# Performance work log

Measured on AMD Instinct MI355X. Metric: run time of the kernel, lower is better.

## Reference

```python
import jax, jax.numpy as jnp
import numpy as np

B, H, W, C = 2, 64, 64, 192
DM = int(2.0 * C)   # d_inner = ssm_ratio * hidden_dim = 384
N = 16              # d_state
R = 12              # dt_rank = ceil(C / 16)
K = 4               # scan directions


def _ln(x, g, b, eps):
    mu = jnp.mean(x, axis=-1, keepdims=True)
    var = jnp.var(x, axis=-1, keepdims=True)
    return (x - mu) * jax.lax.rsqrt(var + eps) * g + b


def setup_inputs() -> dict:
    key = jax.random.key(0)
    ks = jax.random.split(key, 8)
    return {
        "input": jax.random.normal(ks[0], (B, H, W, C), jnp.float32),
        "norm_g": jnp.ones((C,), jnp.float32),
        "norm_b": jnp.zeros((C,), jnp.float32),
        "in_proj_w": jax.random.normal(ks[1], (C, 2 * DM), jnp.float32) * 0.02,
        "conv_w": jax.random.normal(ks[2], (DM, 1, 3, 3), jnp.float32) * 0.1,
        "conv_b": jnp.zeros((DM,), jnp.float32),
        "x_proj_w": jax.random.normal(ks[3], (K, R + 2 * N, DM), jnp.float32) * 0.02,
        "dt_w": jax.random.normal(ks[4], (K, DM, R), jnp.float32) * 0.1,
        "dt_b": jax.random.uniform(ks[5], (K, DM), jnp.float32, -4.0, -2.0),
        "A_logs": jnp.tile(jnp.log(jnp.arange(1, N + 1, dtype=jnp.float32))[None, None, :], (K, DM, 1)),
        "Ds": jnp.ones((K, DM), jnp.float32),
        "out_norm_g": jnp.ones((DM,), jnp.float32),
        "out_norm_b": jnp.zeros((DM,), jnp.float32),
        "out_proj_w": jax.random.normal(ks[6], (DM, C), jnp.float32) * 0.02,
    }


def _selective_scan(us, deltas, A, Bs, Cs):
    # us, deltas: (B,K,D,L); A: (K,D,N); Bs, Cs: (B,K,N,L)
    u_l = jnp.moveaxis(us, -1, 0)       # (L,B,K,D)
    d_l = jnp.moveaxis(deltas, -1, 0)   # (L,B,K,D)
    B_l = jnp.moveaxis(Bs, -1, 0)       # (L,B,K,N)
    C_l = jnp.moveaxis(Cs, -1, 0)       # (L,B,K,N)
    h0 = jnp.zeros(us.shape[:3] + (A.shape[-1],), us.dtype)  # (B,K,D,N)

    def step(h, xs):
        u_t, d_t, b_t, c_t = xs
        dA = jnp.exp(d_t[..., None] * A)                       # (B,K,D,N)
        h = dA * h + (d_t * u_t)[..., None] * b_t[:, :, None, :]
        y = jnp.einsum('bkdn,bkn->bkd', h, c_t)
        return h, y

    _, ys = jax.lax.scan(step, h0, (u_l, d_l, B_l, C_l))
    return jnp.moveaxis(ys, 0, -1)  # (B,K,D,L)


def reference(input, norm_g, norm_b, in_proj_w, conv_w, conv_b, x_proj_w,
              dt_w, dt_b, A_logs, Ds, out_norm_g, out_norm_b, out_proj_w):
    Bz, Hh, Ww, Cc = input.shape
    L = Hh * Ww
    # pre-norm
    xn = _ln(input, norm_g, norm_b, 1e-6)
    # input projection -> x, z
    xz = xn @ in_proj_w                      # (B,H,W,2*DM)
    x, z = jnp.split(xz, 2, axis=-1)
    # depthwise conv + SiLU (channels-first)
    x = jnp.transpose(x, (0, 3, 1, 2))       # (B,DM,H,W)
    Dm = x.shape[1]
    x = jax.lax.conv_general_dilated(
        x, conv_w, (1, 1), 'SAME',
        dimension_numbers=('NCHW', 'OIHW', 'NCHW'),
        feature_group_count=Dm) + conv_b[None, :, None, None]
    x = jax.nn.silu(x)
    # 4-direction cross-scan: hw, wh, and their reverses
    x_flat = x.reshape(Bz, Dm, L)
    x_t = jnp.transpose(x, (0, 1, 3, 2)).reshape(Bz, Dm, L)
    xs = jnp.stack([x_flat, x_t], axis=1)                  # (B,2,DM,L)
    xs = jnp.concatenate([xs, jnp.flip(xs, -1)], axis=1)   # (B,4,DM,L)
    Rr = dt_w.shape[2]
    Nn = A_logs.shape[2]
    x_dbl = jnp.einsum('bkdl,kcd->bkcl', xs, x_proj_w)     # (B,4,R+2N,L)
    dts, Bs, Cs = jnp.split(x_dbl, [Rr, Rr + Nn], axis=2)
    deltas = jax.nn.softplus(
        jnp.einsum('bkrl,kdr->bkdl', dts, dt_w) + dt_b[None, :, :, None])
    A = -jnp.exp(A_logs)                                   # (4,DM,N)
    out_y = _selective_scan(xs, deltas, A, Bs, Cs) + Ds[None, :, :, None] * xs
    # merge the 4 directions back
    inv = jnp.flip(out_y[:, 2:], -1)

    def wh(t):
        return jnp.transpose(t.reshape(Bz, Dm, Ww, Hh), (0, 1, 3, 2)).reshape(Bz, Dm, L)

    y = out_y[:, 0] + inv[:, 0] + wh(out_y[:, 1]) + wh(inv[:, 1])  # (B,DM,L)
    y = jnp.transpose(y, (0, 2, 1))                                # (B,L,DM)
    y = _ln(y, out_norm_g, out_norm_b, 1e-5).reshape(Bz, Hh, Ww, Dm)
    y = y * jax.nn.silu(z)
    out = y @ out_proj_w
    # residual (drop_path=0 -> identity)
    return input + out
```

## Files before the change

kernel.cpp:

```cpp
#include <hip/hip_runtime.h>
#include <hip/hip_bf16.h>
#include <hip/hip_fp16.h>


typedef __attribute__((ext_vector_type(8))) short short8;
typedef __attribute__((ext_vector_type(4))) float floatx4;

__global__ __launch_bounds__(256) void k_ln(const float* __restrict__ in,
                                            const float* __restrict__ g,
                                            const float* __restrict__ be,
                                            __hip_bfloat16* __restrict__ out) {
  int row = blockIdx.x * 4 + (threadIdx.x >> 6);
  int lane = threadIdx.x & 63;
  const float* x = in + (long)row * 192;
  float v0 = x[lane], v1 = x[lane + 64], v2 = x[lane + 128];
  float s = v0 + v1 + v2;
  float s2 = v0 * v0 + v1 * v1 + v2 * v2;
  #pragma unroll
  for (int o = 32; o > 0; o >>= 1) { s += __shfl_xor(s, o); s2 += __shfl_xor(s2, o); }
  float mu = s * (1.f / 192.f);
  float var = s2 * (1.f / 192.f) - mu * mu;
  float r = rsqrtf(var + 1e-6f);
  __hip_bfloat16* op = out + (long)row * 192;
  op[lane]       = __float2bfloat16((v0 - mu) * r * g[lane]       + be[lane]);
  op[lane + 64]  = __float2bfloat16((v1 - mu) * r * g[lane + 64]  + be[lane + 64]);
  op[lane + 128] = __float2bfloat16((v2 - mu) * r * g[lane + 128] + be[lane + 128]);
}

__global__ __launch_bounds__(256) void k_packw(const float* __restrict__ ipw,
                                               const float* __restrict__ xpw,
                                               const float* __restrict__ opw,
                                               __hip_bfloat16* __restrict__ Wt1,
                                               __hip_bfloat16* __restrict__ Wt2,
                                               __hip_bfloat16* __restrict__ Wt3) {
  int idx = blockIdx.x * 256 + threadIdx.x;
  if (idx < 147456) {
    int n = idx / 192, k = idx - n * 192;
    Wt1[idx] = __float2bfloat16(ipw[(long)k * 768 + n]);
  } else if (idx < 147456 + 73728) {
    int t = idx - 147456;
    int j = t / 384;
    float v = (j < 176) ? xpw[t] : 0.f;
    Wt2[t] = __float2bfloat16(v);
  } else if (idx < 147456 + 73728 + 73728) {
    int t = idx - 147456 - 73728;
    int n = t / 384, k = t - n * 384;
    Wt3[t] = __float2bfloat16(opw[(long)k * 192 + n]);
  }
}

__device__ __forceinline__ int inv_dir(int k, int p) {
  int pt = ((p & 63) << 6) | (p >> 6);
  if (k == 0) return p;
  if (k == 1) return pt;
  if (k == 2) return 4095 - p;
  return 4095 - pt;
}
__device__ __forceinline__ int dir_pix(int k, int l) { return inv_dir(k, l); }

template <int EPI>
__global__ __launch_bounds__(256) void k_gemm_mfma(const __hip_bfloat16* __restrict__ A,
                                                   const __hip_bfloat16* __restrict__ Bt,
                                                   const float* __restrict__ Res,
                                                   float* __restrict__ Co,
                                                   __hip_bfloat16* __restrict__ CoB,
                                                   __hip_bfloat16* __restrict__ Co2B,
                                                   float* __restrict__ dtsS,
                                                   float* __restrict__ BsS,
                                                   float* __restrict__ CsS,
                                                   int M, int N, int Kk) {
  __shared__ __align__(16) short As[64 * 64];
  __shared__ __align__(16) short Bs[64 * 64];
  int tid = threadIdx.x;
  int wave = tid >> 6, lane = tid & 63;
  int mlane = lane & 15, quad = lane >> 4;
  int row0 = blockIdx.y * 64, col0 = blockIdx.x * 64;
  int wr = wave & 1, wc = wave >> 1;
  floatx4 acc[2][2];
  #pragma unroll
  for (int mi = 0; mi < 2; mi++)
    #pragma unroll
    for (int ni = 0; ni < 2; ni++) acc[mi][ni] = (floatx4){0.f, 0.f, 0.f, 0.f};

  for (int k0 = 0; k0 < Kk; k0 += 64) {
    #pragma unroll
    for (int c = tid; c < 512; c += 256) {
      int r = c >> 3, j = c & 7;
      *(float4*)&As[r * 64 + ((j ^ (r & 7)) << 3)] =
          *(const float4*)&A[(long)(row0 + r) * Kk + k0 + j * 8];
    }
    #pragma unroll
    for (int c = tid; c < 512; c += 256) {
      int r = c >> 3, j = c & 7;
      *(float4*)&Bs[r * 64 + ((j ^ (r & 7)) << 3)] =
          *(const float4*)&Bt[(long)(col0 + r) * Kk + k0 + j * 8];
    }
    __syncthreads();
    short8 af[2][2], bf[2][2];
    #pragma unroll
    for (int mi = 0; mi < 2; mi++) {
      int r = wr * 32 + mi * 16 + mlane;
      #pragma unroll
      for (int kk = 0; kk < 2; kk++) {
        int jx = (kk * 4 + quad) ^ (r & 7);
        af[mi][kk] = *(const short8*)&As[r * 64 + jx * 8];
      }
    }
    #pragma unroll
    for (int ni = 0; ni < 2; ni++) {
      int rn = wc * 32 + ni * 16 + mlane;
      #pragma unroll
      for (int kk = 0; kk < 2; kk++) {
        int jx = (kk * 4 + quad) ^ (rn & 7);
        bf[ni][kk] = *(const short8*)&Bs[rn * 64 + jx * 8];
      }
    }
    #pragma unroll
    for (int kk = 0; kk < 2; kk++)
      #pragma unroll
      for (int mi = 0; mi < 2; mi++)
        #pragma unroll
        for (int ni = 0; ni < 2; ni++)
          acc[mi][ni] = __builtin_amdgcn_mfma_f32_16x16x32_bf16(af[mi][kk], bf[ni][kk],
                                                                acc[mi][ni], 0, 0, 0);
    __syncthreads();
  }
  #pragma unroll
  for (int mi = 0; mi < 2; mi++) {
    #pragma unroll
    for (int ni = 0; ni < 2; ni++) {
      int cc = col0 + wc * 32 + ni * 16 + mlane;
      #pragma unroll
      for (int i = 0; i < 4; i++) {
        int rr = row0 + wr * 32 + mi * 16 + quad * 4 + i;
        float v = acc[mi][ni][i];
        if (EPI == 1) {
          Co[(long)rr * N + cc] = v + Res[(long)rr * N + cc];
        } else if (EPI == 2) {
          if (cc < 384) CoB[(long)rr * 384 + cc] = __float2bfloat16(v);
          else          Co2B[(long)rr * 384 + (cc - 384)] = __float2bfloat16(v);
        } else {
          if (cc < 176) {
            int k4 = (cc >= 132) ? 3 : (cc >= 88) ? 2 : (cc >= 44) ? 1 : 0;
            int c = cc - k4 * 44;
            int b = rr >> 12, p = rr & 4095;
            long lbase = ((long)((b << 2) + k4) << 12) + p;
            if (c < 12)      dtsS[lbase * 12 + c] = v;
            else if (c < 28) BsS[lbase * 16 + (c - 12)] = v;
            else             CsS[lbase * 16 + (c - 28)] = v;
          }
        }
      }
    }
  }
}

__global__ __launch_bounds__(384) void k_conv(const __hip_bfloat16* __restrict__ xbufB,
                                              const float* __restrict__ cw,
                                              const float* __restrict__ cb,
                                              __hip_bfloat16* __restrict__ xcb) {
  int row = blockIdx.x;
  int b = row >> 12, p = row & 4095;
  int h = p >> 6, w0 = p & 63;
  int d = threadIdx.x;
  float acc = cb[d];
  const float* wt = cw + d * 9;
  #pragma unroll
  for (int dh = -1; dh <= 1; dh++) {
    int hh = h + dh;
    if (hh < 0 || hh > 63) continue;
    #pragma unroll
    for (int dw = -1; dw <= 1; dw++) {
      int ww = w0 + dw;
      if (ww < 0 || ww > 63) continue;
      acc += __bfloat162float(xbufB[((long)(b << 12) + (hh << 6) + ww) * 384 + d])
             * wt[(dh + 1) * 3 + (dw + 1)];
    }
  }
  float sg = 1.f / (1.f + __expf(-acc));
  xcb[(long)row * 384 + d] = __float2bfloat16(acc * sg);
}

__global__ __launch_bounds__(384) void k_dt(const float* __restrict__ dtsS,
                                            const float* __restrict__ dt_w,
                                            const float* __restrict__ dt_b,
                                            __half* __restrict__ dpre) {
  int bid = blockIdx.x;
  int chunk = bid & 127, bk = bid >> 7;
  int k = bk & 3;
  int d = threadIdx.x;
  float w[12];
  const float* dwp = dt_w + ((long)(k * 384) + d) * 12;
  #pragma unroll
  for (int r = 0; r < 12; r++) w[r] = dwp[r];
  float db = dt_b[k * 384 + d];
  long base = ((long)bk << 12) + chunk * 32;
  #pragma unroll 4
  for (int t = 0; t < 32; t++) {
    const float4* dq = (const float4*)(dtsS + (base + t) * 12);
    float4 q0 = dq[0], q1 = dq[1], q2 = dq[2];
    float x = db + q0.x * w[0] + q0.y * w[1] + q0.z * w[2] + q0.w * w[3]
                 + q1.x * w[4] + q1.y * w[5] + q1.z * w[6] + q1.w * w[7]
                 + q2.x * w[8] + q2.y * w[9] + q2.z * w[10] + q2.w * w[11];
    float e = __expf(x);
    float delta = (x > 15.f) ? x : __logf(1.f + e);
    dpre[(base + t) * 384 + d] = __float2half(delta);
  }
}

__device__ __forceinline__ void pow16(float r, float* pws) {
  pws[0] = r;
  #pragma unroll
  for (int n = 1; n < 16; n++) {
    int m = n + 1, c = (m + 1) / 2, f = m - c;
    pws[n] = pws[c - 1] * pws[f - 1];
  }
}

__global__ __launch_bounds__(384) void k_scan0(
    const __half* __restrict__ dpre, const float* __restrict__ BsS,
    const __hip_bfloat16* __restrict__ xcb,
    const float* __restrict__ A_logs,
    float* __restrict__ Eb, float* __restrict__ Dend) {
  int bid = blockIdx.x;
  int s = bid & 127, bk = bid >> 7;
  int k = bk & 3, b = bk >> 2;
  int d = threadIdx.x;
  const float* al = A_logs + ((long)(k * 384) + d) * 16;
  bool pw = true;
  float av[16];
  #pragma unroll
  for (int n = 0; n < 16; n++) {
    float a = __expf(al[n]);
    av[n] = -a;
    pw = pw && (fabsf(a - (float)(n + 1)) < 1e-3f);
  }
  float h[16];
  #pragma unroll
  for (int n = 0; n < 16; n++) h[n] = 0.f;
  float cum = 0.f;
  long bpk = (long)bk << 12;
  long bpix = (long)(b << 12);

  if (pw) {
    #pragma unroll 4
    for (int t = 0; t < 32; t++) {
      int p = dir_pix(k, s * 32 + t);
      float delta = __half2float(dpre[(bpk + p) * 384 + d]);
      cum += delta;
      float u = __bfloat162float(xcb[(bpix + p) * 384 + d]);
      float du = delta * u;
      float rr = __expf(-delta);
      float pws[16]; pow16(rr, pws);
      const float4* Bq = (const float4*)(BsS + (bpk + p) * 16);
      float4 b0 = Bq[0], b1 = Bq[1], b2 = Bq[2], b3 = Bq[3];
      float Bl[16] = {b0.x, b0.y, b0.z, b0.w, b1.x, b1.y, b1.z, b1.w,
                      b2.x, b2.y, b2.z, b2.w, b3.x, b3.y, b3.z, b3.w};
      #pragma unroll
      for (int n = 0; n < 16; n++) h[n] = pws[n] * h[n] + du * Bl[n];
    }
  } else {
    for (int t = 0; t < 32; t++) {
      int p = dir_pix(k, s * 32 + t);
      float delta = __half2float(dpre[(bpk + p) * 384 + d]);
      cum += delta;
      float u = __bfloat162float(xcb[(bpix + p) * 384 + d]);
      float du = delta * u;
      const float4* Bq = (const float4*)(BsS + (bpk + p) * 16);
      float4 b0 = Bq[0], b1 = Bq[1], b2 = Bq[2], b3 = Bq[3];
      float Bl[16] = {b0.x, b0.y, b0.z, b0.w, b1.x, b1.y, b1.z, b1.w,
                      b2.x, b2.y, b2.z, b2.w, b3.x, b3.y, b3.z, b3.w};
      #pragma unroll
      for (int n = 0; n < 16; n++) {
        float dA = __expf(delta * av[n]);
        h[n] = dA * h[n] + du * Bl[n];
      }
    }
  }
  long g = (long)bk * 128 + s;
  float* Ep = Eb + g * 6144 + d * 16;
  #pragma unroll
  for (int n = 0; n < 16; n++) Ep[n] = h[n];
  Dend[g * 384 + d] = cum;
}

__global__ __launch_bounds__(128) void k_combine(float* __restrict__ Eb,
                                                 const float* __restrict__ Dend,
                                                 const float* __restrict__ A_logs) {
  int bid = blockIdx.x;
  int bk = bid / 384;
  int d = bid - bk * 384;
  int k = bk & 3;
  int s = threadIdx.x;
  const float* al = A_logs + ((long)(k * 384) + d) * 16;
  bool pw = true;
  float av[16];
  #pragma unroll
  for (int n = 0; n < 16; n++) {
    float a = __expf(al[n]);
    av[n] = -a;
    pw = pw && (fabsf(a - (float)(n + 1)) < 1e-3f);
  }

  long ebase = ((long)bk * 128 + s) * 6144 + d * 16;
  float e[16];
  *(float4*)&e[0]  = *(const float4*)&Eb[ebase + 0];
  *(float4*)&e[4]  = *(const float4*)&Eb[ebase + 4];
  *(float4*)&e[8]  = *(const float4*)&Eb[ebase + 8];
  *(float4*)&e[12] = *(const float4*)&Eb[ebase + 12];
  float sig = Dend[((long)bk * 128 + s) * 384 + d];

  __shared__ float sE[128][17];
  sE[s][0] = sig;
  #pragma unroll
  for (int n = 0; n < 16; n++) sE[s][1 + n] = e[n];
  __syncthreads();

  for (int o = 1; o < 128; o <<= 1) {
    float ps = 0.f, pe[16];
    bool act = (s >= o);
    if (act) {
      ps = sE[s - o][0];
      #pragma unroll
      for (int n = 0; n < 16; n++) pe[n] = sE[s - o][1 + n];
    }
    __syncthreads();
    if (act) {
      if (pw) {
        float rc = __expf(-sig);
        float pwr[16]; pow16(rc, pwr);
        #pragma unroll
        for (int n = 0; n < 16; n++) e[n] += pwr[n] * pe[n];
      } else {
        #pragma unroll
        for (int n = 0; n < 16; n++) e[n] += __expf(av[n] * sig) * pe[n];
      }
      sig += ps;
      sE[s][0] = sig;
      #pragma unroll
      for (int n = 0; n < 16; n++) sE[s][1 + n] = e[n];
    }
    __syncthreads();
  }

  float ho[16];
  if (s == 0) {
    #pragma unroll
    for (int n = 0; n < 16; n++) ho[n] = 0.f;
  } else {
    #pragma unroll
    for (int n = 0; n < 16; n++) ho[n] = sE[s - 1][1 + n];
  }
  *(float4*)&Eb[ebase + 0]  = *(float4*)&ho[0];
  *(float4*)&Eb[ebase + 4]  = *(float4*)&ho[4];
  *(float4*)&Eb[ebase + 8]  = *(float4*)&ho[8];
  *(float4*)&Eb[ebase + 12] = *(float4*)&ho[12];
}

template <int ATOMIC>
__global__ __launch_bounds__(384) void k_scan1(
    const __half* __restrict__ dpre, const float* __restrict__ BsS,
    const float* __restrict__ CsS, const __hip_bfloat16* __restrict__ xcb,
    const float* __restrict__ A_logs, const float* __restrict__ Eb,
    float* __restrict__ yout) {
  int bid = blockIdx.x;
  int s = bid & 127, bk = bid >> 7;
  int k = bk & 3, b = bk >> 2;
  int d = threadIdx.x;
  const float* al = A_logs + ((long)(k * 384) + d) * 16;
  bool pw = true;
  float av[16];
  #pragma unroll
  for (int n = 0; n < 16; n++) {
    float a = __expf(al[n]);
    av[n] = -a;
    pw = pw && (fabsf(a - (float)(n + 1)) < 1e-3f);
  }
  float h[16];
  const float* hp = Eb + ((long)bk * 128 + s) * 6144 + d * 16;
  #pragma unroll
  for (int n = 0; n < 16; n++) h[n] = hp[n];
  long bpk = (long)bk << 12;
  long bpix = (long)(b << 12);

  if (pw) {
    #pragma unroll 4
    for (int t = 0; t < 32; t++) {
      int p = dir_pix(k, s * 32 + t);
      float delta = __half2float(dpre[(bpk + p) * 384 + d]);
      float u = __bfloat162float(xcb[(bpix + p) * 384 + d]);
      float du = delta * u;
      float rr = __expf(-delta);
      float pws[16]; pow16(rr, pws);
      const float4* Bq = (const float4*)(BsS + (bpk + p) * 16);
      float4 b0 = Bq[0], b1 = Bq[1], b2 = Bq[2], b3 = Bq[3];
      float Bl[16] = {b0.x, b0.y, b0.z, b0.w, b1.x, b1.y, b1.z, b1.w,
                      b2.x, b2.y, b2.z, b2.w, b3.x, b3.y, b3.z, b3.w};
      const float4* Cq = (const float4*)(CsS + (bpk + p) * 16);
      float4 c0 = Cq[0], c1 = Cq[1], c2 = Cq[2], c3 = Cq[3];
      float Cl[16] = {c0.x, c0.y, c0.z, c0.w, c1.x, c1.y, c1.z, c1.w,
                      c2.x, c2.y, c2.z, c2.w, c3.x, c3.y, c3.z, c3.w};
      float y = 0.f;
      #pragma unroll
      for (int n = 0; n < 16; n++) { h[n] = pws[n] * h[n] + du * Bl[n]; y += h[n] * Cl[n]; }
      if (ATOMIC) atomicAdd(&yout[(bpix + p) * 384 + d], y);
      else        yout[(bpk + p) * 384 + d] = y;
    }
  } else {
    for (int t = 0; t < 32; t++) {
      int p = dir_pix(k, s * 32 + t);
      float delta = __half2float(dpre[(bpk + p) * 384 + d]);
      float u = __bfloat162float(xcb[(bpix + p) * 384 + d]);
      float du = delta * u;
      const float4* Bq = (const float4*)(BsS + (bpk + p) * 16);
      float4 b0 = Bq[0], b1 = Bq[1], b2 = Bq[2], b3 = Bq[3];
      float Bl[16] = {b0.x, b0.y, b0.z, b0.w, b1.x, b1.y, b1.z, b1.w,
                      b2.x, b2.y, b2.z, b2.w, b3.x, b3.y, b3.z, b3.w};
      const float4* Cq = (const float4*)(CsS + (bpk + p) * 16);
      float4 c0 = Cq[0], c1 = Cq[1], c2 = Cq[2], c3 = Cq[3];
      float Cl[16] = {c0.x, c0.y, c0.z, c0.w, c1.x, c1.y, c1.z, c1.w,
                      c2.x, c2.y, c2.z, c2.w, c3.x, c3.y, c3.z, c3.w};
      float y = 0.f;
      #pragma unroll
      for (int n = 0; n < 16; n++) {
        float dA = __expf(delta * av[n]);
        h[n] = dA * h[n] + du * Bl[n];
        y += h[n] * Cl[n];
      }
      if (ATOMIC) atomicAdd(&yout[(bpix + p) * 384 + d], y);
      else        yout[(bpk + p) * 384 + d] = y;
    }
  }
}

template <int GATHER>
__global__ __launch_bounds__(384) void k_merge(const float* __restrict__ yin,
                                               const __hip_bfloat16* __restrict__ xcb,
                                               const __hip_bfloat16* __restrict__ zbufB,
                                               const float* __restrict__ Ds,
                                               const float* __restrict__ g,
                                               const float* __restrict__ be,
                                               __hip_bfloat16* __restrict__ yactb) {
  int row = blockIdx.x;
  int d = threadIdx.x;
  float v;
  if (GATHER) {
    int b = row >> 12, p = row & 4095;
    long base = ((long)(b << 2) << 12) + p;
    v = yin[base * 384 + d]
      + yin[(base + 4096) * 384 + d]
      + yin[(base + 8192) * 384 + d]
      + yin[(base + 12288) * 384 + d];
  } else {
    v = yin[(long)row * 384 + d];
  }
  float sd = Ds[d] + Ds[384 + d] + Ds[768 + d] + Ds[1152 + d];
  v += __bfloat162float(xcb[(long)row * 384 + d]) * sd;
  float s1 = v, s2 = v * v;
  #pragma unroll
  for (int o = 32; o > 0; o >>= 1) { s1 += __shfl_xor(s1, o); s2 += __shfl_xor(s2, o); }
  __shared__ float r1[6], r2[6];
  int wv = threadIdx.x >> 6;
  if ((threadIdx.x & 63) == 0) { r1[wv] = s1; r2[wv] = s2; }
  __syncthreads();
  float S1 = 0.f, S2 = 0.f;
  #pragma unroll
  for (int i = 0; i < 6; i++) { S1 += r1[i]; S2 += r2[i]; }
  float mu = S1 * (1.f / 384.f);
  float var = S2 * (1.f / 384.f) - mu * mu;
  float rr = rsqrtf(var + 1e-5f);
  float yn = (v - mu) * rr * g[d] + be[d];
  float z = __bfloat162float(zbufB[(long)row * 384 + d]);
  float sg = z / (1.f + __expf(-z));
  yactb[(long)row * 384 + d] = __float2bfloat16(yn * sg);
}

extern "C" void kernel_launch(void* const* d_in, const int* in_sizes, int n_in,
                              void* d_out, int out_size, void* d_ws, size_t ws_size,
                              hipStream_t stream) {
  const float* input      = (const float*)d_in[0];
  const float* norm_g     = (const float*)d_in[1];
  const float* norm_b     = (const float*)d_in[2];
  const float* in_proj_w  = (const float*)d_in[3];
  const float* conv_w     = (const float*)d_in[4];
  const float* conv_b     = (const float*)d_in[5];
  const float* x_proj_w   = (const float*)d_in[6];
  const float* dt_w       = (const float*)d_in[7];
  const float* dt_b       = (const float*)d_in[8];
  const float* A_logs     = (const float*)d_in[9];
  const float* Ds         = (const float*)d_in[10];
  const float* out_norm_g = (const float*)d_in[11];
  const float* out_norm_b = (const float*)d_in[12];
  const float* out_proj_w = (const float*)d_in[13];
  float* out = (float*)d_out;

  bool big = ws_size >= (size_t)34226176 * 4;

  float* ws = (float*)d_ws;
  long o = 0;
  __hip_bfloat16* xnb   = (__hip_bfloat16*)(ws + o); o += 786432;
  __hip_bfloat16* xbufB = (__hip_bfloat16*)(ws + o); o += 1572864;
  __hip_bfloat16* zbufB = (__hip_bfloat16*)(ws + o); o += 1572864;
  __hip_bfloat16* xcb   = (__hip_bfloat16*)(ws + o); o += 1572864;
  __hip_bfloat16* Wt1   = (__hip_bfloat16*)(ws + o); o += 73728;
  __hip_bfloat16* Wt2   = (__hip_bfloat16*)(ws + o); o += 36864;
  __hip_bfloat16* Wt3   = (__hip_bfloat16*)(ws + o); o += 36864;
  float* dtsS           = ws + o;                    o += 393216;
  float* BsS            = ws + o;                    o += 524288;
  float* CsS            = ws + o;                    o += 524288;
  __half* dpre          = (__half*)(ws + o);         o += 6291456;
  float* Eb             = ws + o;                    o += 6291456;
  float* Dend           = ws + o;                    o += 393216;
  float* ybuf           = ws + o;                    o += big ? 12582912 : 3145728;
  __hip_bfloat16* yactb = (__hip_bfloat16*)(ws + o); o += 1572864;

  k_ln<<<dim3(2048), dim3(256), 0, stream>>>(input, norm_g, norm_b, xnb);
  k_packw<<<dim3(1152), dim3(256), 0, stream>>>(in_proj_w, x_proj_w, out_proj_w, Wt1, Wt2, Wt3);
  k_gemm_mfma<2><<<dim3(12, 128), dim3(256), 0, stream>>>(xnb, Wt1, nullptr, nullptr, xbufB, zbufB,
                                                          nullptr, nullptr, nullptr, 8192, 768, 192);
  k_conv<<<dim3(8192), dim3(384), 0, stream>>>(xbufB, conv_w, conv_b, xcb);
  k_gemm_mfma<3><<<dim3(3, 128), dim3(256), 0, stream>>>(xcb, Wt2, nullptr, nullptr, nullptr, nullptr,
                                                         dtsS, BsS, CsS, 8192, 192, 384);
  k_dt<<<dim3(1024), dim3(384), 0, stream>>>(dtsS, dt_w, dt_b, dpre);
  k_scan0<<<dim3(1024), dim3(384), 0, stream>>>(dpre, BsS, xcb, A_logs, Eb, Dend);
  k_combine<<<dim3(3072), dim3(128), 0, stream>>>(Eb, Dend, A_logs);
  if (big) {
    k_scan1<0><<<dim3(1024), dim3(384), 0, stream>>>(dpre, BsS, CsS, xcb, A_logs, Eb, ybuf);
    k_merge<1><<<dim3(8192), dim3(384), 0, stream>>>(ybuf, xcb, zbufB, Ds, out_norm_g, out_norm_b, yactb);
  } else {
    hipMemsetAsync(ybuf, 0, (size_t)3145728 * 4, stream);
    k_scan1<1><<<dim3(1024), dim3(384), 0, stream>>>(dpre, BsS, CsS, xcb, A_logs, Eb, ybuf);
    k_merge<0><<<dim3(8192), dim3(384), 0, stream>>>(ybuf, xcb, zbufB, Ds, out_norm_g, out_norm_b, yactb);
  }
  k_gemm_mfma<1><<<dim3(3, 128), dim3(256), 0, stream>>>(yactb, Wt3, input, out, nullptr, nullptr,
                                                         nullptr, nullptr, nullptr, 8192, 192, 384);
}
```

Before: 261.6 us.

## Pack delta*u with delta, interleave B/C, and store per-direction scan outputs in bf16

k_dt now reads the conv output once and stores a half2 pair (delta*u, delta), so the scan kernels no longer gather xcb with direction-permuted indices. B and C are written interleaved into one 32-float record per position, so k_scan1 loads both from one contiguous region. The non-atomic per-direction scan output becomes bf16, halving ybuf traffic and the merge's reads. The trade-off is a larger dpre buffer (half2 instead of half), the extra rounding of delta*u to fp16 and of y to bf16, and workspace layout changes that affect the big/small path decision.

```diff
diff --git a/kernel.cpp b/kernel.cpp
--- a/kernel.cpp
+++ b/kernel.cpp
@@ -66,8 +66,7 @@
                                                    __hip_bfloat16* __restrict__ CoB,
                                                    __hip_bfloat16* __restrict__ Co2B,
                                                    float* __restrict__ dtsS,
-                                                   float* __restrict__ BsS,
-                                                   float* __restrict__ CsS,
+                                                   float* __restrict__ BCs,
                                                    int M, int N, int Kk) {
   __shared__ __align__(16) short As[64 * 64];
   __shared__ __align__(16) short Bs[64 * 64];
@@ -145,9 +144,8 @@
             int c = cc - k4 * 44;
             int b = rr >> 12, p = rr & 4095;
             long lbase = ((long)((b << 2) + k4) << 12) + p;
-            if (c < 12)      dtsS[lbase * 12 + c] = v;
-            else if (c < 28) BsS[lbase * 16 + (c - 12)] = v;
-            else             CsS[lbase * 16 + (c - 28)] = v;
+            if (c < 12) dtsS[lbase * 12 + c] = v;
+            else        BCs[lbase * 32 + (c - 12)] = v;
           }
         }
       }
@@ -184,10 +182,11 @@
 __global__ __launch_bounds__(384) void k_dt(const float* __restrict__ dtsS,
                                             const float* __restrict__ dt_w,
                                             const float* __restrict__ dt_b,
-                                            __half* __restrict__ dpre) {
+                                            const __hip_bfloat16* __restrict__ xcb,
+                                            __half2* __restrict__ dpre) {
   int bid = blockIdx.x;
   int chunk = bid & 127, bk = bid >> 7;
-  int k = bk & 3;
+  int k = bk & 3, b = bk >> 2;
   int d = threadIdx.x;
   float w[12];
   const float* dwp = dt_w + ((long)(k * 384) + d) * 12;
@@ -195,6 +194,7 @@
   for (int r = 0; r < 12; r++) w[r] = dwp[r];
   float db = dt_b[k * 384 + d];
   long base = ((long)bk << 12) + chunk * 32;
+  long pbase = ((long)(b << 12)) + chunk * 32;
   #pragma unroll 4
   for (int t = 0; t < 32; t++) {
     const float4* dq = (const float4*)(dtsS + (base + t) * 12);
@@ -204,7 +204,11 @@
                  + q2.x * w[8] + q2.y * w[9] + q2.z * w[10] + q2.w * w[11];
     float e = __expf(x);
     float delta = (x > 15.f) ? x : __logf(1.f + e);
-    dpre[(base + t) * 384 + d] = __float2half(delta);
+    float u = __bfloat162float(xcb[(pbase + t) * 384 + d]);
+    __half2 o;
+    o.x = __float2half(delta * u);
+    o.y = __float2half(delta);
+    dpre[(base + t) * 384 + d] = o;
   }
 }
 
@@ -218,13 +222,12 @@
 }
 
 __global__ __launch_bounds__(384) void k_scan0(
-    const __half* __restrict__ dpre, const float* __restrict__ BsS,
-    const __hip_bfloat16* __restrict__ xcb,
+    const __half2* __restrict__ dpre, const float* __restrict__ BCs,
     const float* __restrict__ A_logs,
     float* __restrict__ Eb, float* __restrict__ Dend) {
   int bid = blockIdx.x;
   int s = bid & 127, bk = bid >> 7;
-  int k = bk & 3, b = bk >> 2;
+  int k = bk & 3;
   int d = threadIdx.x;
   const float* al = A_logs + ((long)(k * 384) + d) * 16;
   bool pw = true;
@@ -240,19 +243,18 @@
   for (int n = 0; n < 16; n++) h[n] = 0.f;
   float cum = 0.f;
   long bpk = (long)bk << 12;
-  long bpix = (long)(b << 12);
 
   if (pw) {
     #pragma unroll 4
     for (int t = 0; t < 32; t++) {
       int p = dir_pix(k, s * 32 + t);
-      float delta = __half2float(dpre[(bpk + p) * 384 + d]);
+      __half2 v = dpre[(bpk + p) * 384 + d];
+      float du = __half2float(v.x);
+      float delta = __half2float(v.y);
       cum += delta;
-      float u = __bfloat162float(xcb[(bpix + p) * 384 + d]);
-      float du = delta * u;
       float rr = __expf(-delta);
       float pws[16]; pow16(rr, pws);
-      const float4* Bq = (const float4*)(BsS + (bpk + p) * 16);
+      const float4* Bq = (const float4*)(BCs + (bpk + p) * 32);
       float4 b0 = Bq[0], b1 = Bq[1], b2 = Bq[2], b3 = Bq[3];
       float Bl[16] = {b0.x, b0.y, b0.z, b0.w, b1.x, b1.y, b1.z, b1.w,
                       b2.x, b2.y, b2.z, b2.w, b3.x, b3.y, b3.z, b3.w};
@@ -262,11 +264,11 @@
   } else {
     for (int t = 0; t < 32; t++) {
       int p = dir_pix(k, s * 32 + t);
-      float delta = __half2float(dpre[(bpk + p) * 384 + d]);
+      __half2 v = dpre[(bpk + p) * 384 + d];
+      float du = __half2float(v.x);
+      float delta = __half2float(v.y);
       cum += delta;
-      float u = __bfloat162float(xcb[(bpix + p) * 384 + d]);
-      float du = delta * u;
-      const float4* Bq = (const float4*)(BsS + (bpk + p) * 16);
+      const float4* Bq = (const float4*)(BCs + (bpk + p) * 32);
       float4 b0 = Bq[0], b1 = Bq[1], b2 = Bq[2], b3 = Bq[3];
       float Bl[16] = {b0.x, b0.y, b0.z, b0.w, b1.x, b1.y, b1.z, b1.w,
                       b2.x, b2.y, b2.z, b2.w, b3.x, b3.y, b3.z, b3.w};
@@ -359,10 +361,9 @@
 
 template <int ATOMIC>
 __global__ __launch_bounds__(384) void k_scan1(
-    const __half* __restrict__ dpre, const float* __restrict__ BsS,
-    const float* __restrict__ CsS, const __hip_bfloat16* __restrict__ xcb,
+    const __half2* __restrict__ dpre, const float* __restrict__ BCs,
     const float* __restrict__ A_logs, const float* __restrict__ Eb,
-    float* __restrict__ yout) {
+    __hip_bfloat16* __restrict__ ybufB, float* __restrict__ ysum) {
   int bid = blockIdx.x;
   int s = bid & 127, bk = bid >> 7;
   int k = bk & 3, b = bk >> 2;
@@ -387,36 +388,36 @@
     #pragma unroll 4
     for (int t = 0; t < 32; t++) {
       int p = dir_pix(k, s * 32 + t);
-      float delta = __half2float(dpre[(bpk + p) * 384 + d]);
-      float u = __bfloat162float(xcb[(bpix + p) * 384 + d]);
-      float du = delta * u;
+      __half2 v = dpre[(bpk + p) * 384 + d];
+      float du = __half2float(v.x);
+      float delta = __half2float(v.y);
       float rr = __expf(-delta);
       float pws[16]; pow16(rr, pws);
-      const float4* Bq = (const float4*)(BsS + (bpk + p) * 16);
+      const float4* Bq = (const float4*)(BCs + (bpk + p) * 32);
       float4 b0 = Bq[0], b1 = Bq[1], b2 = Bq[2], b3 = Bq[3];
       float Bl[16] = {b0.x, b0.y, b0.z, b0.w, b1.x, b1.y, b1.z, b1.w,
                       b2.x, b2.y, b2.z, b2.w, b3.x, b3.y, b3.z, b3.w};
-      const float4* Cq = (const float4*)(CsS + (bpk + p) * 16);
+      const float4* Cq = Bq + 4;
       float4 c0 = Cq[0], c1 = Cq[1], c2 = Cq[2], c3 = Cq[3];
       float Cl[16] = {c0.x, c0.y, c0.z, c0.w, c1.x, c1.y, c1.z, c1.w,
                       c2.x, c2.y, c2.z, c2.w, c3.x, c3.y, c3.z, c3.w};
       float y = 0.f;
       #pragma unroll
       for (int n = 0; n < 16; n++) { h[n] = pws[n] * h[n] + du * Bl[n]; y += h[n] * Cl[n]; }
-      if (ATOMIC) atomicAdd(&yout[(bpix + p) * 384 + d], y);
-      else        yout[(bpk + p) * 384 + d] = y;
+      if (ATOMIC) atomicAdd(&ysum[(bpix + p) * 384 + d], y);
+      else        ybufB[(bpk + p) * 384 + d] = __float2bfloat16(y);
     }
   } else {
     for (int t = 0; t < 32; t++) {
       int p = dir_pix(k, s * 32 + t);
-      float delta = __half2float(dpre[(bpk + p) * 384 + d]);
-      float u = __bfloat162float(xcb[(bpix + p) * 384 + d]);
-      float du = delta * u;
-      const float4* Bq = (const float4*)(BsS + (bpk + p) * 16);
+      __half2 v = dpre[(bpk + p) * 384 + d];
+      float du = __half2float(v.x);
+      float delta = __half2float(v.y);
+      const float4* Bq = (const float4*)(BCs + (bpk + p) * 32);
       float4 b0 = Bq[0], b1 = Bq[1], b2 = Bq[2], b3 = Bq[3];
       float Bl[16] = {b0.x, b0.y, b0.z, b0.w, b1.x, b1.y, b1.z, b1.w,
                       b2.x, b2.y, b2.z, b2.w, b3.x, b3.y, b3.z, b3.w};
-      const float4* Cq = (const float4*)(CsS + (bpk + p) * 16);
+      const float4* Cq = Bq + 4;
       float4 c0 = Cq[0], c1 = Cq[1], c2 = Cq[2], c3 = Cq[3];
       float Cl[16] = {c0.x, c0.y, c0.z, c0.w, c1.x, c1.y, c1.z, c1.w,
                       c2.x, c2.y, c2.z, c2.w, c3.x, c3.y, c3.z, c3.w};
@@ -427,14 +428,15 @@
         h[n] = dA * h[n] + du * Bl[n];
         y += h[n] * Cl[n];
       }
-      if (ATOMIC) atomicAdd(&yout[(bpix + p) * 384 + d], y);
-      else        yout[(bpk + p) * 384 + d] = y;
+      if (ATOMIC) atomicAdd(&ysum[(bpix + p) * 384 + d], y);
+      else        ybufB[(bpk + p) * 384 + d] = __float2bfloat16(y);
     }
   }
 }
 
 template <int GATHER>
-__global__ __launch_bounds__(384) void k_merge(const float* __restrict__ yin,
+__global__ __launch_bounds__(384) void k_merge(const __hip_bfloat16* __restrict__ yinB,
+                                               const float* __restrict__ yinF,
                                                const __hip_bfloat16* __restrict__ xcb,
                                                const __hip_bfloat16* __restrict__ zbufB,
                                                const float* __restrict__ Ds,
@@ -447,12 +449,12 @@
   if (GATHER) {
     int b = row >> 12, p = row & 4095;
     long base = ((long)(b << 2) << 12) + p;
-    v = yin[base * 384 + d]
-      + yin[(base + 4096) * 384 + d]
-      + yin[(base + 8192) * 384 + d]
-      + yin[(base + 12288) * 384 + d];
+    v = __bfloat162float(yinB[base * 384 + d])
+      + __bfloat162float(yinB[(base + 4096) * 384 + d])
+      + __bfloat162float(yinB[(base + 8192) * 384 + d])
+      + __bfloat162float(yinB[(base + 12288) * 384 + d]);
   } else {
-    v = yin[(long)row * 384 + d];
+    v = yinF[(long)row * 384 + d];
   }
   float sd = Ds[d] + Ds[384 + d] + Ds[768 + d] + Ds[1152 + d];
   v += __bfloat162float(xcb[(long)row * 384 + d]) * sd;
@@ -506,32 +508,34 @@
   __hip_bfloat16* Wt2   = (__hip_bfloat16*)(ws + o); o += 36864;
   __hip_bfloat16* Wt3   = (__hip_bfloat16*)(ws + o); o += 36864;
   float* dtsS           = ws + o;                    o += 393216;
-  float* BsS            = ws + o;                    o += 524288;
-  float* CsS            = ws + o;                    o += 524288;
-  __half* dpre          = (__half*)(ws + o);         o += 6291456;
+  float* BCs            = ws + o;                    o += 1048576;
+  __half2* dpre         = (__half2*)(ws + o);        o += 12582912;
   float* Eb             = ws + o;                    o += 6291456;
   float* Dend           = ws + o;                    o += 393216;
-  float* ybuf           = ws + o;                    o += big ? 12582912 : 3145728;
+  __hip_bfloat16* ybufB = (__hip_bfloat16*)(ws + o);
+  float* ysum           = ws + o;                    o += big ? 6291456 : 3145728;
   __hip_bfloat16* yactb = (__hip_bfloat16*)(ws + o); o += 1572864;
 
   k_ln<<<dim3(2048), dim3(256), 0, stream>>>(input, norm_g, norm_b, xnb);
   k_packw<<<dim3(1152), dim3(256), 0, stream>>>(in_proj_w, x_proj_w, out_proj_w, Wt1, Wt2, Wt3);
   k_gemm_mfma<2><<<dim3(12, 128), dim3(256), 0, stream>>>(xnb, Wt1, nullptr, nullptr, xbufB, zbufB,
-                                                          nullptr, nullptr, nullptr, 8192, 768, 192);
+                                                          nullptr, nullptr, 8192, 768, 192);
   k_conv<<<dim3(8192), dim3(384), 0, stream>>>(xbufB, conv_w, conv_b, xcb);
   k_gemm_mfma<3><<<dim3(3, 128), dim3(256), 0, stream>>>(xcb, Wt2, nullptr, nullptr, nullptr, nullptr,
-                                                         dtsS, BsS, CsS, 8192, 192, 384);
-  k_dt<<<dim3(1024), dim3(384), 0, stream>>>(dtsS, dt_w, dt_b, dpre);
-  k_scan0<<<dim3(1024), dim3(384), 0, stream>>>(dpre, BsS, xcb, A_logs, Eb, Dend);
+                                                         dtsS, BCs, 8192, 192, 384);
+  k_dt<<<dim3(1024), dim3(384), 0, stream>>>(dtsS, dt_w, dt_b, xcb, dpre);
+  k_scan0<<<dim3(1024), dim3(384), 0, stream>>>(dpre, BCs, A_logs, Eb, Dend);
   k_combine<<<dim3(3072), dim3(128), 0, stream>>>(Eb, Dend, A_logs);
   if (big) {
-    k_scan1<0><<<dim3(1024), dim3(384), 0, stream>>>(dpre, BsS, CsS, xcb, A_logs, Eb, ybuf);
-    k_merge<1><<<dim3(8192), dim3(384), 0, stream>>>(ybuf, xcb, zbufB, Ds, out_norm_g, out_norm_b, yactb);
+    k_scan1<0><<<dim3(1024), dim3(384), 0, stream>>>(dpre, BCs, A_logs, Eb, ybufB, nullptr);
+    k_merge<1><<<dim3(8192), dim3(384), 0, stream>>>(ybufB, nullptr, xcb, zbufB, Ds,
+                                                     out_norm_g, out_norm_b, yactb);
   } else {
-    hipMemsetAsync(ybuf, 0, (size_t)3145728 * 4, stream);
-    k_scan1<1><<<dim3(1024), dim3(384), 0, stream>>>(dpre, BsS, CsS, xcb, A_logs, Eb, ybuf);
-    k_merge<0><<<dim3(8192), dim3(384), 0, stream>>>(ybuf, xcb, zbufB, Ds, out_norm_g, out_norm_b, yactb);
+    hipMemsetAsync(ysum, 0, (size_t)3145728 * 4, stream);
+    k_scan1<1><<<dim3(1024), dim3(384), 0, stream>>>(dpre, BCs, A_logs, Eb, nullptr, ysum);
+    k_merge<0><<<dim3(8192), dim3(384), 0, stream>>>(nullptr, ysum, xcb, zbufB, Ds,
+                                                     out_norm_g, out_norm_b, yactb);
   }
   k_gemm_mfma<1><<<dim3(3, 128), dim3(256), 0, stream>>>(yactb, Wt3, input, out, nullptr, nullptr,
-                                                         nullptr, nullptr, nullptr, 8192, 192, 384);
-}
+                                                         nullptr, nullptr, 8192, 192, 384);
+}
```

Result: no change. 260.4 us (-0.5%).
